# Kernel tuning notes

Measured on AMD Instinct MI355X. Metric: run time of the kernel, lower is better.

Reference implementation:

```python
import jax, jax.numpy as jnp
import numpy as np

T, B, D, H = 2048, 2, 1024, 16
NH, DH = H // 2, D // H   # 8 heads per direction, d_head = 64
DFF = 4096


def layer_norm(x, g, b, eps=1e-5):
    mu = jnp.mean(x, axis=-1, keepdims=True)
    var = jnp.mean(jnp.square(x - mu), axis=-1, keepdims=True)
    return (x - mu) * jax.lax.rsqrt(var + eps) * g + b


def rel_shift(x):
    # x: [q, k, b, n] -> Transformer-XL relative shift
    q, k, b, n = x.shape
    x = jnp.concatenate([jnp.zeros((q, 1, b, n), x.dtype), x], axis=1)
    return x.reshape(k + 1, q, b, n)[1:].reshape(q, k, b, n)


def rel_attn(w, r, mask, qkv_w, r_w, r_w_bias, r_r_bias):
    # w: [T, B, D], r: [R, 1, D], mask: [T, T] bool (True = masked)
    t, b, _ = w.shape
    heads = jnp.einsum('tbd,ed->tbe', w, qkv_w)              # [T,B,3*NH*DH]
    q, k, v = jnp.split(heads, 3, axis=-1)
    q = q.reshape(t, b, NH, DH)
    k = k.reshape(t, b, NH, DH)
    v = v.reshape(t, b, NH, DH)
    rk = jnp.einsum('rd,ed->re', r[:, 0, :], r_w).reshape(-1, NH, DH)  # [R,NH,DH]
    AC = jnp.einsum('ibnd,jbnd->ijbn', q + r_w_bias, k)
    BD = rel_shift(jnp.einsum('ibnd,jnd->ijbn', q + r_r_bias, rk))
    score = (AC + BD) * (1.0 / np.sqrt(DH))
    score = jnp.where(mask[:, :, None, None], jnp.finfo(score.dtype).min, score)
    prob = jax.nn.softmax(score, axis=1)
    vec = jnp.einsum('ijbn,jbnd->ibnd', prob, v)
    return vec.reshape(t, b, NH * DH)


def setup_inputs() -> dict:
    key = jax.random.key(0)
    ks = jax.random.split(key, 24)
    s = 0.02
    causal = jnp.triu(jnp.ones((T, T), dtype=bool), k=1)
    return {
        'x': jax.random.normal(ks[0], (T, B, D), jnp.float32),
        'pos': jax.random.normal(ks[1], (T, 1, D), jnp.float32),
        'mask_fwd': causal,
        'mask_bwd': causal,
        'ln1_g': jnp.ones((D,), jnp.float32), 'ln1_b': jnp.zeros((D,), jnp.float32),
        'ln2_g': jnp.ones((D,), jnp.float32), 'ln2_b': jnp.zeros((D,), jnp.float32),
        'ln3_g': jnp.ones((D,), jnp.float32), 'ln3_b': jnp.zeros((D,), jnp.float32),
        'qkv_f': jax.random.normal(ks[2], (3 * NH * DH, D), jnp.float32) * s,
        'rnet_f': jax.random.normal(ks[3], (NH * DH, D), jnp.float32) * s,
        'rwb_f': jax.random.normal(ks[4], (NH, DH), jnp.float32) * s,
        'rrb_f': jax.random.normal(ks[5], (NH, DH), jnp.float32) * s,
        'qkv_b': jax.random.normal(ks[6], (3 * NH * DH, D), jnp.float32) * s,
        'rnet_b': jax.random.normal(ks[7], (NH * DH, D), jnp.float32) * s,
        'rwb_b': jax.random.normal(ks[8], (NH, DH), jnp.float32) * s,
        'rrb_b': jax.random.normal(ks[9], (NH, DH), jnp.float32) * s,
        'wo': jax.random.normal(ks[10], (D, D), jnp.float32) * s,
        'bo': jnp.zeros((D,), jnp.float32),
        'w1': jax.random.normal(ks[11], (DFF, D), jnp.float32) * s,
        'b1': jnp.zeros((DFF,), jnp.float32),
        'w2': jax.random.normal(ks[12], (D, DFF), jnp.float32) * s,
        'b2': jnp.zeros((D,), jnp.float32),
    }


def reference(x, pos, mask_fwd, mask_bwd,
              ln1_g, ln1_b, ln2_g, ln2_b, ln3_g, ln3_b,
              qkv_f, rnet_f, rwb_f, rrb_f,
              qkv_b, rnet_b, rwb_b, rrb_b,
              wo, bo, w1, b1, w2, b2):
    # --- bidirectional relative attention ---
    q_fwd = layer_norm(x, ln1_g, ln1_b)
    q_bwd = layer_norm(jnp.flip(x, axis=0), ln2_g, ln2_b)
    out_fwd = rel_attn(q_fwd, pos, mask_fwd, qkv_f, rnet_f, rwb_f, rrb_f)
    out_bwd = rel_attn(q_bwd, pos, mask_bwd, qkv_b, rnet_b, rwb_b, rrb_b)
    out = jnp.concatenate([out_fwd, jnp.flip(out_bwd, axis=0)], axis=-1)
    out = jnp.einsum('tbd,ed->tbe', out, wo) + bo
    h = x + out                     # postprocess_attn: dropout(id) + residual
    # --- feed forward: LN -> Linear -> ReLU -> Linear -> residual ---
    y = layer_norm(h, ln3_g, ln3_b)
    y = jax.nn.relu(jnp.einsum('tbd,fd->tbf', y, w1) + b1)
    y = jnp.einsum('tbf,df->tbd', y, w2) + b2
    return h + y
```

## Files before the change

### kernel.cpp

```cpp
#include <hip/hip_runtime.h>
#include <cstdint>
#include <cstddef>


typedef unsigned short ushort_t;
typedef __bf16 bf16x8 __attribute__((ext_vector_type(8)));
typedef float f32x4 __attribute__((ext_vector_type(4)));
typedef unsigned short us8 __attribute__((ext_vector_type(8)));
typedef unsigned short us4 __attribute__((ext_vector_type(4)));

#define DEV static __device__ __forceinline__

DEV ushort_t f2bf(float x) {
  union { float f; unsigned u; } v; v.f = x;
  unsigned r = (v.u + 0x7FFFu + ((v.u >> 16) & 1u)) >> 16;
  return (ushort_t)r;
}
DEV ushort_t f2bt(float x) {
  union { float f; unsigned u; } v; v.f = x;
  return (ushort_t)(v.u >> 16);
}
DEV float bf2f(ushort_t h) {
  union { unsigned u; float f; } v; v.u = ((unsigned)h) << 16;
  return v.f;
}
DEV float fexp2(float x) { float r; asm("v_exp_f32 %0, %1" : "=v"(r) : "v"(x)); return r; }
DEV f32x4 mfma16(bf16x8 a, bf16x8 b, f32x4 c) {
  return __builtin_amdgcn_mfma_f32_16x16x32_bf16(a, b, c, 0, 0, 0);
}
DEV void gld16(const void* g, void* l) {
  __builtin_amdgcn_global_load_lds((const __attribute__((address_space(1))) void*)g,
                                   (__attribute__((address_space(3))) void*)l,
                                   16, 0, 0);
}

constexpr float SCLQ = 0.125f * 1.44269504088896f;

constexpr size_t O_QKV_F  = 0;
constexpr size_t O_QKV_B  = 3145728;
constexpr size_t O_RNET_F = 6291456;
constexpr size_t O_RNET_B = 7340032;
constexpr size_t O_WO     = 8388608;
constexpr size_t O_W1     = 10485760;
constexpr size_t O_W2     = 18874368;
constexpr size_t O_RKREV_F= 27262976;
constexpr size_t O_RKREV_B= 29360128;
constexpr size_t O_QAC_F  = 31457280;
constexpr size_t O_QBD_F  = 35651584;
constexpr size_t O_KK_F   = 39845888;
constexpr size_t O_VT_F   = 44040192;
constexpr size_t O_QAC_B  = 48234496;
constexpr size_t O_QBD_B  = 52428800;
constexpr size_t O_KK_B   = 56623104;
constexpr size_t O_VT_B   = 60817408;
constexpr size_t O_H      = 65011712;
constexpr size_t O_LN3    = 81788928;
constexpr size_t ZONE     = 90177536;
constexpr size_t O_POS    = ZONE + 0;
constexpr size_t O_LN1    = ZONE + 4194304;
constexpr size_t O_LN2    = ZONE + 12582912;
constexpr size_t O_HEADS_F= ZONE + 20971520;
constexpr size_t O_HEADS_B= ZONE + 33554432;
constexpr size_t O_ACAT   = ZONE + 0;
constexpr size_t O_FFNM   = ZONE + 8388608;
constexpr size_t O_FPART  = O_QAC_F;

struct PrepArgs {
  const float* src[8];
  ushort_t* dst[8];
  int bstart[8];
  int cvt_blocks;
  const float* x;
  const float* g1; const float* b1;
  const float* g2; const float* b2;
  ushort_t* o1; ushort_t* o2;
};
__global__ __launch_bounds__(256)
void prep_k(PrepArgs a) {
  __shared__ float sbuf[8];
  const int bx = blockIdx.x;
  const int tid = threadIdx.x;
  if (bx < a.cvt_blocks) {
    int s = 0;
#pragma unroll
    for (int k = 1; k < 8; ++k) if (bx >= a.bstart[k]) s = k;
    int i = (bx - a.bstart[s]) * 256 + tid;
    float4 v = reinterpret_cast<const float4*>(a.src[s])[i];
    us4 o; o[0] = f2bf(v.x); o[1] = f2bf(v.y); o[2] = f2bf(v.z); o[3] = f2bf(v.w);
    reinterpret_cast<us4*>(a.dst[s])[i] = o;
    return;
  }
  const int row = bx - a.cvt_blocks;
  const float* xr = a.x + (size_t)row * 1024;
  float4 v = reinterpret_cast<const float4*>(xr)[tid];
  float s  = v.x + v.y + v.z + v.w;
  float s2 = v.x*v.x + v.y*v.y + v.z*v.z + v.w*v.w;
  for (int m = 32; m >= 1; m >>= 1) { s += __shfl_xor(s, m, 64); s2 += __shfl_xor(s2, m, 64); }
  int w = tid >> 6;
  if ((tid & 63) == 0) { sbuf[w] = s; sbuf[4 + w] = s2; }
  __syncthreads();
  float S  = sbuf[0] + sbuf[1] + sbuf[2] + sbuf[3];
  float S2 = sbuf[4] + sbuf[5] + sbuf[6] + sbuf[7];
  float mu  = S * (1.f / 1024.f);
  float var = S2 * (1.f / 1024.f) - mu * mu;
  float inv = rsqrtf(var + 1e-5f);
  int t = row >> 1, b = row & 1;
  size_t r2 = ((size_t)(2047 - t) * 2 + b) * 1024;
  float4 G1 = reinterpret_cast<const float4*>(a.g1)[tid];
  float4 B1 = reinterpret_cast<const float4*>(a.b1)[tid];
  float4 G2 = reinterpret_cast<const float4*>(a.g2)[tid];
  float4 B2 = reinterpret_cast<const float4*>(a.b2)[tid];
  float n0 = (v.x - mu) * inv, n1 = (v.y - mu) * inv, n2 = (v.z - mu) * inv, n3 = (v.w - mu) * inv;
  us4 aa, c;
  aa[0] = f2bf(n0 * G1.x + B1.x); aa[1] = f2bf(n1 * G1.y + B1.y);
  aa[2] = f2bf(n2 * G1.z + B1.z); aa[3] = f2bf(n3 * G1.w + B1.w);
  c[0] = f2bf(n0 * G2.x + B2.x); c[1] = f2bf(n1 * G2.y + B2.y);
  c[2] = f2bf(n2 * G2.z + B2.z); c[3] = f2bf(n3 * G2.w + B2.w);
  reinterpret_cast<us4*>(a.o1 + (size_t)row * 1024)[tid] = aa;
  reinterpret_cast<us4*>(a.o2 + r2)[tid] = c;
}

__global__ __launch_bounds__(256)
void ln_one_k(const float* __restrict__ x,
              const float* __restrict__ g1, const float* __restrict__ b1,
              ushort_t* __restrict__ o1) {
  __shared__ float sbuf[8];
  const int row = blockIdx.x;
  const int tid = threadIdx.x;
  const float* xr = x + (size_t)row * 1024;
  float4 v = reinterpret_cast<const float4*>(xr)[tid];
  float s  = v.x + v.y + v.z + v.w;
  float s2 = v.x*v.x + v.y*v.y + v.z*v.z + v.w*v.w;
  for (int m = 32; m >= 1; m >>= 1) { s += __shfl_xor(s, m, 64); s2 += __shfl_xor(s2, m, 64); }
  int w = tid >> 6;
  if ((tid & 63) == 0) { sbuf[w] = s; sbuf[4 + w] = s2; }
  __syncthreads();
  float S  = sbuf[0] + sbuf[1] + sbuf[2] + sbuf[3];
  float S2 = sbuf[4] + sbuf[5] + sbuf[6] + sbuf[7];
  float mu  = S * (1.f / 1024.f);
  float var = S2 * (1.f / 1024.f) - mu * mu;
  float inv = rsqrtf(var + 1e-5f);
  float4 G1 = reinterpret_cast<const float4*>(g1)[tid];
  float4 B1 = reinterpret_cast<const float4*>(b1)[tid];
  us4 a;
  a[0] = f2bf((v.x - mu) * inv * G1.x + B1.x);
  a[1] = f2bf((v.y - mu) * inv * G1.y + B1.y);
  a[2] = f2bf((v.z - mu) * inv * G1.z + B1.z);
  a[3] = f2bf((v.w - mu) * inv * G1.w + B1.w);
  reinterpret_cast<us4*>(o1 + (size_t)row * 1024)[tid] = a;
}

template <int EPI>
__global__ __launch_bounds__(256)
void gemm_bt(const ushort_t* __restrict__ A, const ushort_t* __restrict__ B,
             void* __restrict__ C, const float* __restrict__ bias,
             const float* __restrict__ resid, int M, int N, int K) {
  __shared__ ushort_t As[128 * 64];
  __shared__ ushort_t Bs[128 * 64];
  const int tid = threadIdx.x;
  const int lane = tid & 63;
  const int w = tid >> 6;
  const int wm = w >> 1, wn = w & 1;
  const int row0 = blockIdx.y * 128, col0 = blockIdx.x * 128;
  const int lr = lane & 15;
  const int lkb = (lane >> 4) * 8;
  const int rr = lane >> 3;
  const int scb = ((lane & 7) ^ rr) * 8;
  const f32x4 fz = {0.f, 0.f, 0.f, 0.f};
  f32x4 acc[4][4];
#pragma unroll
  for (int i = 0; i < 4; ++i)
#pragma unroll
    for (int j = 0; j < 4; ++j) acc[i][j] = fz;

  for (int k0 = 0; k0 < K; k0 += 64) {
    __syncthreads();
#pragma unroll
    for (int it = 0; it < 4; ++it) {
      int rbase = it * 32 + w * 8;
      gld16(A + (size_t)(row0 + rbase + rr) * K + k0 + scb, (char*)As + rbase * 128);
      gld16(B + (size_t)(col0 + rbase + rr) * K + k0 + scb, (char*)Bs + rbase * 128);
    }
    __syncthreads();
#pragma unroll
    for (int kk = 0; kk < 64; kk += 32) {
      bf16x8 af[4], bfr[4];
#pragma unroll
      for (int mi = 0; mi < 4; ++mi) {
        int r = wm * 64 + mi * 16 + lr;
        int off = (r * 128 + (kk + lkb) * 2) ^ ((r & 7) << 4);
        af[mi] = *reinterpret_cast<const bf16x8*>((char*)As + off);
      }
#pragma unroll
      for (int ni = 0; ni < 4; ++ni) {
        int r = wn * 64 + ni * 16 + lr;
        int off = (r * 128 + (kk + lkb) * 2) ^ ((r & 7) << 4);
        bfr[ni] = *reinterpret_cast<const bf16x8*>((char*)Bs + off);
      }
#pragma unroll
      for (int mi = 0; mi < 4; ++mi)
#pragma unroll
        for (int ni = 0; ni < 4; ++ni)
          acc[mi][ni] = mfma16(af[mi], bfr[ni], acc[mi][ni]);
    }
  }
#pragma unroll
  for (int mi = 0; mi < 4; ++mi)
#pragma unroll
    for (int ni = 0; ni < 4; ++ni)
#pragma unroll
      for (int r = 0; r < 4; ++r) {
        int row = row0 + wm * 64 + mi * 16 + (lane >> 4) * 4 + r;
        int col = col0 + wn * 64 + ni * 16 + lr;
        float v = acc[mi][ni][r];
        if (EPI == 0) {
          ((ushort_t*)C)[(size_t)row * N + col] = f2bf(v);
        } else if (EPI == 1) {
          v += bias[col]; v = v > 0.f ? v : 0.f;
          ((ushort_t*)C)[(size_t)row * N + col] = f2bf(v);
        } else {
          v += bias[col] + resid[(size_t)row * N + col];
          ((float*)C)[(size_t)row * N + col] = v;
        }
      }
}

__global__ __launch_bounds__(256)
void qkvrk_k(const ushort_t* __restrict__ A0, const ushort_t* __restrict__ A1,
             const ushort_t* __restrict__ A2,
             const ushort_t* __restrict__ B0, const ushort_t* __restrict__ B1,
             const ushort_t* __restrict__ B2, const ushort_t* __restrict__ B3,
             char* __restrict__ wsb,
             const float* __restrict__ rw0, const float* __restrict__ rr0,
             const float* __restrict__ rw1, const float* __restrict__ rr1) {
  const int z = blockIdx.z;
  if (z >= 2 && (blockIdx.x >= 4 || blockIdx.y >= 16)) return;
  const ushort_t* A = (z == 0) ? A0 : (z == 1) ? A1 : A2;
  const ushort_t* B = (z == 0) ? B0 : (z == 1) ? B1 : (z == 2) ? B2 : B3;

  __shared__ ushort_t As[128 * 64];
  __shared__ ushort_t Bs[128 * 64];
  const int tid = threadIdx.x;
  const int lane = tid & 63;
  const int w = tid >> 6;
  const int wm = w >> 1, wn = w & 1;
  const int row0 = blockIdx.y * 128, col0 = blockIdx.x * 128;
  const int lr = lane & 15;
  const int lkb = (lane >> 4) * 8;
  const int rr = lane >> 3;
  const int scb = ((lane & 7) ^ rr) * 8;
  const f32x4 fz = {0.f, 0.f, 0.f, 0.f};
  f32x4 acc[4][4];
#pragma unroll
  for (int i = 0; i < 4; ++i)
#pragma unroll
    for (int j = 0; j < 4; ++j) acc[i][j] = fz;

  for (int k0 = 0; k0 < 1024; k0 += 64) {
    __syncthreads();
#pragma unroll
    for (int it = 0; it < 4; ++it) {
      int rbase = it * 32 + w * 8;
      gld16(A + (size_t)(row0 + rbase + rr) * 1024 + k0 + scb, (char*)As + rbase * 128);
      gld16(B + (size_t)(col0 + rbase + rr) * 1024 + k0 + scb, (char*)Bs + rbase * 128);
    }
    __syncthreads();
#pragma unroll
    for (int kk = 0; kk < 64; kk += 32) {
      bf16x8 af[4], bfr[4];
#pragma unroll
      for (int mi = 0; mi < 4; ++mi) {
        int r = wm * 64 + mi * 16 + lr;
        int off = (r * 128 + (kk + lkb) * 2) ^ ((r & 7) << 4);
        af[mi] = *reinterpret_cast<const bf16x8*>((char*)As + off);
      }
#pragma unroll
      for (int ni = 0; ni < 4; ++ni) {
        int r = wn * 64 + ni * 16 + lr;
        int off = (r * 128 + (kk + lkb) * 2) ^ ((r & 7) << 4);
        bfr[ni] = *reinterpret_cast<const bf16x8*>((char*)Bs + off);
      }
#pragma unroll
      for (int mi = 0; mi < 4; ++mi)
#pragma unroll
        for (int ni = 0; ni < 4; ++ni)
          acc[mi][ni] = mfma16(af[mi], bfr[ni], acc[mi][ni]);
    }
  }
  const int dirz = z & 1;
  const float* rwb = dirz ? rw1 : rw0;
  const float* rrb = dirz ? rr1 : rr0;
#pragma unroll
  for (int mi = 0; mi < 4; ++mi)
#pragma unroll
    for (int ni = 0; ni < 4; ++ni)
#pragma unroll
      for (int r = 0; r < 4; ++r) {
        int row = row0 + wm * 64 + mi * 16 + (lane >> 4) * 4 + r;
        int col = col0 + wn * 64 + ni * 16 + lr;
        float v = acc[mi][ni][r];
        if (z < 2) {
          int t = row >> 1, bb = row & 1;
          if (col < 512) {
            int nn = col >> 6, dh = col & 63;
            ushort_t* q_ac = (ushort_t*)(wsb + (dirz ? O_QAC_B : O_QAC_F));
            ushort_t* q_bd = (ushort_t*)(wsb + (dirz ? O_QBD_B : O_QBD_F));
            size_t o = ((size_t)(bb * 8 + nn) * 2048 + t) * 64 + dh;
            q_ac[o] = f2bf((v + rwb[col]) * SCLQ);
            q_bd[o] = f2bf((v + rrb[col]) * SCLQ);
          } else if (col < 1024) {
            int cc = col - 512;
            int nn = cc >> 6, dh = cc & 63;
            ushort_t* kout = (ushort_t*)(wsb + (dirz ? O_KK_B : O_KK_F));
            kout[((size_t)(bb * 8 + nn) * 2048 + t) * 64 + dh] = f2bf(v);
          } else {
            ushort_t* hv = (ushort_t*)(wsb + (dirz ? O_HEADS_B : O_HEADS_F));
            hv[(size_t)row * 1536 + col] = f2bf(v);
          }
        } else {
          ushort_t* rkrev = (ushort_t*)(wsb + (dirz ? O_RKREV_B : O_RKREV_F));
          int nn = col >> 6, dh = col & 63;
          rkrev[((size_t)nn * 2048 + (2047 - row)) * 64 + dh] = f2bf(v);
        }
      }
}

template <int EPI>
__global__ __launch_bounds__(256)
void gemm_bt2(const ushort_t* __restrict__ A0, const ushort_t* __restrict__ A1,
              const ushort_t* __restrict__ B0, const ushort_t* __restrict__ B1,
              void* __restrict__ C0, void* __restrict__ C1,
              int M, int N, int K, int lda, int ldb) {
  __shared__ ushort_t As[128 * 64];
  __shared__ ushort_t Bs[128 * 64];
  const ushort_t* A = blockIdx.z ? A1 : A0;
  const ushort_t* B = blockIdx.z ? B1 : B0;
  void* C = blockIdx.z ? (void*)C1 : (void*)C0;
  const int tid = threadIdx.x;
  const int lane = tid & 63;
  const int w = tid >> 6;
  const int wm = w >> 1, wn = w & 1;
  const int row0 = blockIdx.y * 128, col0 = blockIdx.x * 128;
  const int lr = lane & 15;
  const int lkb = (lane >> 4) * 8;
  const int rr = lane >> 3;
  const int scb = ((lane & 7) ^ rr) * 8;
  const f32x4 fz = {0.f, 0.f, 0.f, 0.f};
  f32x4 acc[4][4];
#pragma unroll
  for (int i = 0; i < 4; ++i)
#pragma unroll
    for (int j = 0; j < 4; ++j) acc[i][j] = fz;

  for (int k0 = 0; k0 < K; k0 += 64) {
    __syncthreads();
#pragma unroll
    for (int it = 0; it < 4; ++it) {
      int rbase = it * 32 + w * 8;
      gld16(A + (size_t)(row0 + rbase + rr) * lda + k0 + scb, (char*)As + rbase * 128);
      gld16(B + (size_t)(col0 + rbase + rr) * ldb + k0 + scb, (char*)Bs + rbase * 128);
    }
    __syncthreads();
#pragma unroll
    for (int kk = 0; kk < 64; kk += 32) {
      bf16x8 af[4], bfr[4];
#pragma unroll
      for (int mi = 0; mi < 4; ++mi) {
        int r = wm * 64 + mi * 16 + lr;
        int off = (r * 128 + (kk + lkb) * 2) ^ ((r & 7) << 4);
        af[mi] = *reinterpret_cast<const bf16x8*>((char*)As + off);
      }
#pragma unroll
      for (int ni = 0; ni < 4; ++ni) {
        int r = wn * 64 + ni * 16 + lr;
        int off = (r * 128 + (kk + lkb) * 2) ^ ((r & 7) << 4);
        bfr[ni] = *reinterpret_cast<const bf16x8*>((char*)Bs + off);
      }
#pragma unroll
      for (int mi = 0; mi < 4; ++mi)
#pragma unroll
        for (int ni = 0; ni < 4; ++ni)
          acc[mi][ni] = mfma16(af[mi], bfr[ni], acc[mi][ni]);
    }
  }
#pragma unroll
  for (int mi = 0; mi < 4; ++mi)
#pragma unroll
    for (int ni = 0; ni < 4; ++ni)
#pragma unroll
      for (int r = 0; r < 4; ++r) {
        int row = row0 + wm * 64 + mi * 16 + (lane >> 4) * 4 + r;
        int col = col0 + wn * 64 + ni * 16 + lr;
        float v = acc[mi][ni][r];
        if (EPI == 5) ((float*)C)[(size_t)row * N + col] = v;
      }
}

template <int EPI>
__global__ __launch_bounds__(256)
void gemm64(const ushort_t* __restrict__ A0, const ushort_t* __restrict__ A1,
            const ushort_t* __restrict__ B0, const ushort_t* __restrict__ B1,
            void* __restrict__ C0, void* __restrict__ C1,
            const float* __restrict__ bias, const float* __restrict__ resid,
            int M, int N, int K) {
  __shared__ ushort_t As[64 * 64];
  __shared__ ushort_t Bs[128 * 64];
  const ushort_t* A = blockIdx.z ? A1 : A0;
  const ushort_t* B = blockIdx.z ? B1 : B0;
  void* C = blockIdx.z ? (void*)C1 : (void*)C0;
  const int tid = threadIdx.x;
  const int lane = tid & 63;
  const int w = tid >> 6;
  const int wm = w >> 1, wn = w & 1;
  const int row0 = blockIdx.y * 64, col0 = blockIdx.x * 128;
  const int lr = lane & 15;
  const int lkb = (lane >> 4) * 8;
  const int rr = lane >> 3;
  const int scb = ((lane & 7) ^ rr) * 8;
  const f32x4 fz = {0.f, 0.f, 0.f, 0.f};
  f32x4 acc[2][4];
#pragma unroll
  for (int i = 0; i < 2; ++i)
#pragma unroll
    for (int j = 0; j < 4; ++j) acc[i][j] = fz;

  for (int k0 = 0; k0 < K; k0 += 64) {
    __syncthreads();
#pragma unroll
    for (int it = 0; it < 2; ++it) {
      int rbase = it * 32 + w * 8;
      gld16(A + (size_t)(row0 + rbase + rr) * K + k0 + scb, (char*)As + rbase * 128);
    }
#pragma unroll
    for (int it = 0; it < 4; ++it) {
      int rbase = it * 32 + w * 8;
      gld16(B + (size_t)(col0 + rbase + rr) * K + k0 + scb, (char*)Bs + rbase * 128);
    }
    __syncthreads();
#pragma unroll
    for (int kk = 0; kk < 64; kk += 32) {
      bf16x8 af[2], bfr[4];
#pragma unroll
      for (int mi = 0; mi < 2; ++mi) {
        int r = wm * 32 + mi * 16 + lr;
        int off = (r * 128 + (kk + lkb) * 2) ^ ((r & 7) << 4);
        af[mi] = *reinterpret_cast<const bf16x8*>((char*)As + off);
      }
#pragma unroll
      for (int ni = 0; ni < 4; ++ni) {
        int r = wn * 64 + ni * 16 + lr;
        int off = (r * 128 + (kk + lkb) * 2) ^ ((r & 7) << 4);
        bfr[ni] = *reinterpret_cast<const bf16x8*>((char*)Bs + off);
      }
#pragma unroll
      for (int mi = 0; mi < 2; ++mi)
#pragma unroll
        for (int ni = 0; ni < 4; ++ni)
          acc[mi][ni] = mfma16(af[mi], bfr[ni], acc[mi][ni]);
    }
  }
#pragma unroll
  for (int mi = 0; mi < 2; ++mi)
#pragma unroll
    for (int ni = 0; ni < 4; ++ni)
#pragma unroll
      for (int r = 0; r < 4; ++r) {
        int row = row0 + wm * 32 + mi * 16 + (lane >> 4) * 4 + r;
        int col = col0 + wn * 64 + ni * 16 + lr;
        float v = acc[mi][ni][r];
        if (EPI == 2) {
          v += bias[col] + resid[(size_t)row * N + col];
          ((float*)C)[(size_t)row * N + col] = v;
        }
      }
}

__global__ __launch_bounds__(256)
void ffn2_red_k(const float* __restrict__ p0, const float* __restrict__ p1,
                const float* __restrict__ b2, const float* __restrict__ h,
                float* __restrict__ out) {
  const int row = blockIdx.x;
  const int tid = threadIdx.x;
  const size_t base = (size_t)row * 1024;
  float4 a = reinterpret_cast<const float4*>(p0 + base)[tid];
  float4 b = reinterpret_cast<const float4*>(p1 + base)[tid];
  float4 hv = reinterpret_cast<const float4*>(h + base)[tid];
  float4 bb = reinterpret_cast<const float4*>(b2)[tid];
  float4 o;
  o.x = a.x + b.x + hv.x + bb.x;
  o.y = a.y + b.y + hv.y + bb.y;
  o.z = a.z + b.z + hv.z + bb.z;
  o.w = a.w + b.w + hv.w + bb.w;
  reinterpret_cast<float4*>(out + base)[tid] = o;
}

__global__ __launch_bounds__(256)
void v_trans2_k(const ushort_t* __restrict__ hf, const ushort_t* __restrict__ hb2,
                char* __restrict__ wsb) {
  __shared__ float tile[64][65];
  const int dir = blockIdx.z;
  const ushort_t* heads = dir ? hb2 : hf;
  ushort_t* vt = (ushort_t*)(wsb + (dir ? O_VT_B : O_VT_F));
  int tt0 = blockIdx.x * 64;
  int bn = blockIdx.y;
  int b = bn >> 3, n = bn & 7;
  int tid = threadIdx.x;
#pragma unroll
  for (int i = 0; i < 16; ++i) {
    int rr = i * 4 + (tid >> 6);
    int cc = tid & 63;
    tile[rr][cc] = bf2f(heads[(size_t)((tt0 + rr) * 2 + b) * 1536 + 1024 + n * 64 + cc]);
  }
  __syncthreads();
#pragma unroll
  for (int i = 0; i < 16; ++i) {
    int dh = i * 4 + (tid >> 6);
    int tt = tid & 63;
    vt[((size_t)bn * 64 + dh) * 2048 + tt0 + tt] = f2bf(tile[tt][dh]);
  }
}

__global__ __launch_bounds__(256)
void attn_k(const char* __restrict__ wsb, ushort_t* __restrict__ outp) {
  __shared__ ushort_t Kbuf[2][64 * 64];
  __shared__ ushort_t Vbuf[2][64 * 64];
  __shared__ alignas(16) ushort_t Gs[4][16 * 84];
  __shared__ ushort_t Ps[4][1024];

  const int tid = threadIdx.x;
  const int lane = tid & 63;
  const int w = tid >> 6;
  const int il = lane & 15;
  const int g = lane >> 4;
  const int lkb = g * 8;
  const int rr = lane >> 3;
  const int scb = ((lane & 7) ^ rr) * 8;

  const int id = (int)(blockIdx.x + (blockIdx.y << 4) + (blockIdx.z << 8));
  const int xcd = id & 7;
  const int ord = id >> 3;
  const int pair = xcd * 4 + (ord & 3);
  const int bx = ord >> 2;
  const int bn = pair & 15;
  const int dir = pair >> 4;

  const ushort_t* qac  = (const ushort_t*)(wsb + (dir ? O_QAC_B : O_QAC_F));
  const ushort_t* qbd  = (const ushort_t*)(wsb + (dir ? O_QBD_B : O_QBD_F));
  const ushort_t* kkv  = (const ushort_t*)(wsb + (dir ? O_KK_B  : O_KK_F));
  const ushort_t* vtp  = (const ushort_t*)(wsb + (dir ? O_VT_B  : O_VT_F));
  const ushort_t* rkrev= (const ushort_t*)(wsb + (dir ? O_RKREV_B : O_RKREV_F));
  const int colbase = dir ? 512 : 0;

  const size_t hb = (size_t)bn * 2048;
  const size_t vbase = (size_t)bn * 64;
  const size_t nb = (size_t)(bn & 7) * 2048;
  const int b = bn >> 3;
  const int n = bn & 7;

  ushort_t* gw = Gs[w];
  char* pw = (char*)Ps[w];

  for (int half = 0; half < 2; ++half) {
    const int it = half ? bx : (31 - bx);
    const int i0 = it * 64;
    const int NT = it + 1;
    const int iw0 = i0 + w * 16;

    auto STAGE = [&](int bi, int j0) {
      ushort_t* kb = Kbuf[bi] + w * 512;
      ushort_t* vbp = Vbuf[bi] + w * 512;
      gld16(kkv + (hb + j0 + w * 8 + rr) * 64 + scb, kb);
      gld16(kkv + (hb + j0 + 32 + w * 8 + rr) * 64 + scb, kb + 2048);
      gld16(vtp + (vbase + w * 8 + rr) * 2048 + j0 + scb, vbp);
      gld16(vtp + (vbase + 32 + w * 8 + rr) * 2048 + j0 + scb, vbp + 2048);
    };

    bf16x8 qa[2], qb[2];
#pragma unroll
    for (int kf = 0; kf < 2; ++kf) {
      size_t off = (hb + iw0 + il) * 64 + kf * 32 + lkb;
      qa[kf] = *reinterpret_cast<const bf16x8*>(qac + off);
      qb[kf] = *reinterpret_cast<const bf16x8*>(qbd + off);
    }

    const f32x4 fz = {0.f, 0.f, 0.f, 0.f};
    f32x4 Oa[4];
#pragma unroll
    for (int nf = 0; nf < 4; ++nf) Oa[nf] = fz;
    float lsum = 0.f;

    STAGE(0, 0);
    __syncthreads();
    int cur = 0;
    for (int jt = 0; jt < NT; ++jt) {
      const int j0 = jt * 64;

      bf16x8 bd0[5], bd1[5];
      const int dbase = iw0 - j0 - 63;
#pragma unroll
      for (int ng = 0; ng < 5; ++ng) {
        int d = dbase + ng * 16 + il;
        d = d < 0 ? 0 : (d > 2047 ? 2047 : d);
        const ushort_t* bp = rkrev + (nb + d) * 64 + lkb;
        bd0[ng] = *reinterpret_cast<const bf16x8*>(bp);
        bd1[ng] = *reinterpret_cast<const bf16x8*>(bp + 32);
      }
      if (jt + 1 < NT) STAGE(cur ^ 1, j0 + 64);

      const ushort_t* Ks = Kbuf[cur];
      const ushort_t* Vs = Vbuf[cur];
      f32x4 S[4], G[5];
#pragma unroll
      for (int nf = 0; nf < 4; ++nf) S[nf] = fz;
#pragma unroll
      for (int ng = 0; ng < 5; ++ng) G[ng] = fz;
      __builtin_amdgcn_s_setprio(1);
#pragma unroll
      for (int kf = 0; kf < 2; ++kf)
#pragma unroll
        for (int nf = 0; nf < 4; ++nf) {
          int r = nf * 16 + il;
          int off = (r * 128 + (kf * 32 + lkb) * 2) ^ ((r & 7) << 4);
          S[nf] = mfma16(*reinterpret_cast<const bf16x8*>((char*)Ks + off), qa[kf], S[nf]);
        }
#pragma unroll
      for (int ng = 0; ng < 5; ++ng) {
        G[ng] = mfma16(bd0[ng], qb[0], G[ng]);
        G[ng] = mfma16(bd1[ng], qb[1], G[ng]);
      }
      __builtin_amdgcn_s_setprio(0);
#pragma unroll
      for (int ng = 0; ng < 5; ++ng) {
        us4 pk;
        pk[0] = f2bt(G[ng][0]); pk[1] = f2bt(G[ng][1]);
        pk[2] = f2bt(G[ng][2]); pk[3] = f2bt(G[ng][3]);
        *reinterpret_cast<us4*>(gw + il * 84 + ng * 16 + g * 4) = pk;
      }
      const bool full = (j0 + 63 <= iw0);
#pragma unroll
      for (int nf = 0; nf < 4; ++nf) {
        int c3 = il - (nf * 16 + g * 4 + 3) + 63;
        int base4 = c3 & ~3;
        int o = c3 & 3;
        const ushort_t* gp = gw + il * 84 + base4;
        uint64_t av = *reinterpret_cast<const uint64_t*>(gp);
        uint64_t bv2 = *reinterpret_cast<const uint64_t*>(gp + 4);
        uint64_t vv = o ? ((av >> (16 * o)) | (bv2 << (64 - 16 * o))) : av;
#pragma unroll
        for (int r = 0; r < 4; ++r) {
          int jl = nf * 16 + g * 4 + r;
          float sv = S[nf][r] + bf2f((ushort_t)(vv >> (16 * (3 - r))));
          if (!full) sv = (j0 + jl <= iw0 + il) ? sv : -1e30f;
          S[nf][r] = sv;
        }
      }
#pragma unroll
      for (int nf = 0; nf < 4; ++nf) {
        us4 pk;
#pragma unroll
        for (int r = 0; r < 4; ++r) {
          float p = fexp2(S[nf][r]);
          lsum += p;
          pk[r] = f2bt(p);
        }
        int off = (il * 128 + (nf * 16 + g * 4) * 2) ^ ((il & 7) << 4);
        *reinterpret_cast<us4*>(pw + off) = pk;
      }
      __builtin_amdgcn_s_setprio(1);
#pragma unroll
      for (int kf = 0; kf < 2; ++kf) {
        int poff = (il * 128 + (kf * 32 + lkb) * 2) ^ ((il & 7) << 4);
        bf16x8 pt = *reinterpret_cast<const bf16x8*>(pw + poff);
#pragma unroll
        for (int nf = 0; nf < 4; ++nf) {
          int r = nf * 16 + il;
          int voff = (r * 128 + (kf * 32 + lkb) * 2) ^ ((r & 7) << 4);
          Oa[nf] = mfma16(*reinterpret_cast<const bf16x8*>((char*)Vs + voff), pt, Oa[nf]);
        }
      }
      __builtin_amdgcn_s_setprio(0);
      __syncthreads();
      cur ^= 1;
    }
    lsum += __shfl_xor(lsum, 16, 64);
    lsum += __shfl_xor(lsum, 32, 64);
    float invl = 1.f / lsum;
    int ig = iw0 + il;
    int tout = dir ? (2047 - ig) : ig;
    size_t orow = ((size_t)tout * 2 + b) * 1024 + colbase + n * 64;
#pragma unroll
    for (int nf = 0; nf < 4; ++nf) {
      us4 pk;
#pragma unroll
      for (int r = 0; r < 4; ++r) pk[r] = f2bf(Oa[nf][r] * invl);
      *reinterpret_cast<us4*>(outp + orow + nf * 16 + g * 4) = pk;
    }
  }
}

extern "C" void kernel_launch(void* const* d_in, const int* in_sizes, int n_in,
                              void* d_out, int out_size, void* d_ws, size_t ws_size,
                              hipStream_t stream) {
  (void)in_sizes; (void)n_in; (void)out_size; (void)ws_size;
  const float* x    = (const float*)d_in[0];
  const float* pos  = (const float*)d_in[1];
  const float* ln1g = (const float*)d_in[4];
  const float* ln1b = (const float*)d_in[5];
  const float* ln2g = (const float*)d_in[6];
  const float* ln2b = (const float*)d_in[7];
  const float* ln3g = (const float*)d_in[8];
  const float* ln3b = (const float*)d_in[9];
  const float* qkvf = (const float*)d_in[10];
  const float* rnetf= (const float*)d_in[11];
  const float* rwbf = (const float*)d_in[12];
  const float* rrbf = (const float*)d_in[13];
  const float* qkvb = (const float*)d_in[14];
  const float* rnetb= (const float*)d_in[15];
  const float* rwbb = (const float*)d_in[16];
  const float* rrbb = (const float*)d_in[17];
  const float* wo   = (const float*)d_in[18];
  const float* bo   = (const float*)d_in[19];
  const float* w1   = (const float*)d_in[20];
  const float* b1   = (const float*)d_in[21];
  const float* w2   = (const float*)d_in[22];
  const float* b2   = (const float*)d_in[23];
  float* out = (float*)d_out;
  char* ws = (char*)d_ws;
  auto U = [&](size_t off) { return (ushort_t*)(ws + off); };

  PrepArgs pa;
  const float* srcs[8] = {qkvf, qkvb, rnetf, rnetb, wo, w1, w2, pos};
  size_t dsts[8] = {O_QKV_F, O_QKV_B, O_RNET_F, O_RNET_B, O_WO, O_W1, O_W2, O_POS};
  int bl[8] = {1536, 1536, 512, 512, 1024, 4096, 4096, 2048};
  int cum = 0;
  for (int s = 0; s < 8; ++s) {
    pa.src[s] = srcs[s];
    pa.dst[s] = U(dsts[s]);
    pa.bstart[s] = cum;
    cum += bl[s];
  }
  pa.cvt_blocks = cum;
  pa.x = x; pa.g1 = ln1g; pa.b1 = ln1b; pa.g2 = ln2g; pa.b2 = ln2b;
  pa.o1 = U(O_LN1); pa.o2 = U(O_LN2);
  prep_k<<<dim3(cum + 4096), dim3(256), 0, stream>>>(pa);

  qkvrk_k<<<dim3(12, 32, 4), dim3(256), 0, stream>>>(
      U(O_LN1), U(O_LN2), U(O_POS),
      U(O_QKV_F), U(O_QKV_B), U(O_RNET_F), U(O_RNET_B),
      ws, rwbf, rrbf, rwbb, rrbb);

  v_trans2_k<<<dim3(32, 16, 2), dim3(256), 0, stream>>>(U(O_HEADS_F), U(O_HEADS_B), ws);

  attn_k<<<dim3(16, 16, 2), dim3(256), 0, stream>>>(ws, U(O_ACAT));

  gemm64<2><<<dim3(8, 64, 1), dim3(256), 0, stream>>>(
      U(O_ACAT), U(O_ACAT), U(O_WO), U(O_WO), ws + O_H, ws + O_H,
      bo, x, 4096, 1024, 1024);

  ln_one_k<<<dim3(4096), dim3(256), 0, stream>>>((const float*)(ws + O_H), ln3g, ln3b, U(O_LN3));
  gemm_bt<1><<<dim3(32, 32), dim3(256), 0, stream>>>(U(O_LN3), U(O_W1), U(O_FFNM), b1, nullptr, 4096, 4096, 1024);

  float* part0 = (float*)(ws + O_FPART);
  float* part1 = part0 + (size_t)4096 * 1024;
  gemm_bt2<5><<<dim3(8, 32, 2), dim3(256), 0, stream>>>(
      U(O_FFNM), U(O_FFNM) + 2048, U(O_W2), U(O_W2) + 2048, part0, part1,
      4096, 1024, 2048, 4096, 4096);
  ffn2_red_k<<<dim3(4096), dim3(256), 0, stream>>>(
      part0, part1, b2, (const float*)(ws + O_H), out);
}
```

Baseline: 311.0 us.

## Flatten qkv grid to skip idle blocks and store FFN2 partials as bf16

The QKV/rk projection launch moves from a 3D grid, where many z>=2 blocks exited at once, to a 1D grid of exactly the needed 896 blocks. Each block decodes its z and tile indices from blockIdx.x. The split-K FFN2 partial sums are now written as bf16 instead of fp32, which halves the write and reread traffic in the reduction kernel. The cost is extra rounding error on the partial sums before they are added together.

```diff
diff --git a/kernel.cpp b/kernel.cpp
--- a/kernel.cpp
+++ b/kernel.cpp
@@ -233,8 +233,20 @@
              char* __restrict__ wsb,
              const float* __restrict__ rw0, const float* __restrict__ rr0,
              const float* __restrict__ rw1, const float* __restrict__ rr1) {
-  const int z = blockIdx.z;
-  if (z >= 2 && (blockIdx.x >= 4 || blockIdx.y >= 16)) return;
+  const int id = (int)blockIdx.x;
+  int z, bxx, byy;
+  if (id < 768) {
+    z = id / 384;
+    int rem = id - z * 384;
+    bxx = rem % 12;
+    byy = rem / 12;
+  } else {
+    int id2 = id - 768;
+    z = 2 + (id2 >> 6);
+    int rem = id2 & 63;
+    bxx = rem & 3;
+    byy = rem >> 2;
+  }
   const ushort_t* A = (z == 0) ? A0 : (z == 1) ? A1 : A2;
   const ushort_t* B = (z == 0) ? B0 : (z == 1) ? B1 : (z == 2) ? B2 : B3;
 
@@ -244,7 +256,7 @@
   const int lane = tid & 63;
   const int w = tid >> 6;
   const int wm = w >> 1, wn = w & 1;
-  const int row0 = blockIdx.y * 128, col0 = blockIdx.x * 128;
+  const int row0 = byy * 128, col0 = bxx * 128;
   const int lr = lane & 15;
   const int lkb = (lane >> 4) * 8;
   const int rr = lane >> 3;
@@ -392,7 +404,7 @@
         int row = row0 + wm * 64 + mi * 16 + (lane >> 4) * 4 + r;
         int col = col0 + wn * 64 + ni * 16 + lr;
         float v = acc[mi][ni][r];
-        if (EPI == 5) ((float*)C)[(size_t)row * N + col] = v;
+        if (EPI == 5) ((ushort_t*)C)[(size_t)row * N + col] = f2bf(v);
       }
 }
 
@@ -476,21 +488,21 @@
 }
 
 __global__ __launch_bounds__(256)
-void ffn2_red_k(const float* __restrict__ p0, const float* __restrict__ p1,
+void ffn2_red_k(const ushort_t* __restrict__ p0, const ushort_t* __restrict__ p1,
                 const float* __restrict__ b2, const float* __restrict__ h,
                 float* __restrict__ out) {
   const int row = blockIdx.x;
   const int tid = threadIdx.x;
   const size_t base = (size_t)row * 1024;
-  float4 a = reinterpret_cast<const float4*>(p0 + base)[tid];
-  float4 b = reinterpret_cast<const float4*>(p1 + base)[tid];
+  us4 a = reinterpret_cast<const us4*>(p0 + base)[tid];
+  us4 b = reinterpret_cast<const us4*>(p1 + base)[tid];
   float4 hv = reinterpret_cast<const float4*>(h + base)[tid];
   float4 bb = reinterpret_cast<const float4*>(b2)[tid];
   float4 o;
-  o.x = a.x + b.x + hv.x + bb.x;
-  o.y = a.y + b.y + hv.y + bb.y;
-  o.z = a.z + b.z + hv.z + bb.z;
-  o.w = a.w + b.w + hv.w + bb.w;
+  o.x = bf2f(a[0]) + bf2f(b[0]) + hv.x + bb.x;
+  o.y = bf2f(a[1]) + bf2f(b[1]) + hv.y + bb.y;
+  o.z = bf2f(a[2]) + bf2f(b[2]) + hv.z + bb.z;
+  o.w = bf2f(a[3]) + bf2f(b[3]) + hv.w + bb.w;
   reinterpret_cast<float4*>(out + base)[tid] = o;
 }
 
@@ -744,7 +756,7 @@
   pa.o1 = U(O_LN1); pa.o2 = U(O_LN2);
   prep_k<<<dim3(cum + 4096), dim3(256), 0, stream>>>(pa);
 
-  qkvrk_k<<<dim3(12, 32, 4), dim3(256), 0, stream>>>(
+  qkvrk_k<<<dim3(896), dim3(256), 0, stream>>>(
       U(O_LN1), U(O_LN2), U(O_POS),
       U(O_QKV_F), U(O_QKV_B), U(O_RNET_F), U(O_RNET_B),
       ws, rwbf, rrbf, rwbb, rrbb);
@@ -760,8 +772,8 @@
   ln_one_k<<<dim3(4096), dim3(256), 0, stream>>>((const float*)(ws + O_H), ln3g, ln3b, U(O_LN3));
   gemm_bt<1><<<dim3(32, 32), dim3(256), 0, stream>>>(U(O_LN3), U(O_W1), U(O_FFNM), b1, nullptr, 4096, 4096, 1024);
 
-  float* part0 = (float*)(ws + O_FPART);
-  float* part1 = part0 + (size_t)4096 * 1024;
+  ushort_t* part0 = U(O_FPART);
+  ushort_t* part1 = U(O_FPART + 8388608);
   gemm_bt2<5><<<dim3(8, 32, 2), dim3(256), 0, stream>>>(
       U(O_FFNM), U(O_FFNM) + 2048, U(O_W2), U(O_W2) + 2048, part0, part1,
       4096, 1024, 2048, 4096, 4096);
```

Result: no change. 306.6 us (median of 2 runs) (-1.4%).
